# Kernel optimization log

Hardware: AMD Instinct MI355X
Metric: run time of the kernel (lower is better)

Reference implementation:

```python
import jax, jax.numpy as jnp
import numpy as np

N_NODES = 140000   # 14 frames * 10000 nodes/frame
N_EDGES = 2240000  # avg degree 16
NFEAT = 128
NHID = 128
N_FRAMES = 14


def setup_inputs() -> dict:
    key = jax.random.key(0)
    k1, k2, k3, k4, k5 = jax.random.split(key, 5)
    x = jax.random.normal(k1, (N_NODES, NFEAT), dtype=jnp.float32)
    # gc1 parameters (only layer actually used in forward)
    W = jax.random.normal(k2, (NFEAT, NHID), dtype=jnp.float32) * 0.05
    b = jnp.zeros((NHID,), dtype=jnp.float32)
    # sparse normalized adjacency as COO edge list (row sorted for fast segment_sum)
    edge_row = jnp.sort(jax.random.randint(k3, (N_EDGES,), 0, N_NODES, dtype=jnp.int32))
    edge_col = jax.random.randint(k4, (N_EDGES,), 0, N_NODES, dtype=jnp.int32)
    edge_val = jax.random.uniform(k5, (N_EDGES,), dtype=jnp.float32)
    return {"x": x, "W": W, "b": b, "edge_val": edge_val,
            "edge_row": edge_row, "edge_col": edge_col}


def reference(x, W, b, edge_val, edge_row, edge_col):
    # GraphConvolution: adj @ (x @ W) + b  (adj sparse, COO)
    support = x @ W                                   # [N, NHID]
    msgs = edge_val[:, None] * support[edge_col]      # [E, NHID] gather
    agg = jax.ops.segment_sum(msgs, edge_row, num_segments=N_NODES,
                              indices_are_sorted=True)  # [N, NHID] scatter-add
    h = jax.nn.relu(agg + b)
    # view(14, -1, c) then max over frame axis
    h = h.reshape(N_FRAMES, -1, NHID)                 # [14, N/14, NHID]
    h = jnp.max(h, axis=0)                            # [N/14, NHID]
    return jax.nn.log_softmax(h, axis=1)
```

## Files before the change

### kernel.cpp

```cpp
#include <hip/hip_runtime.h>
#include <hip/hip_bf16.h>

#define N_NODES 140000
#define N_EDGES 2240000
#define NFEAT 128
#define NHID 128
#define N_FRAMES 14
#define NODES_PER_FRAME 10000
#define CAP 352

typedef __attribute__((ext_vector_type(8))) short frag_b16;
typedef __attribute__((ext_vector_type(4))) int frag_i4;
typedef __attribute__((ext_vector_type(4))) float f32x4;

__device__ __forceinline__ unsigned short f2bf(float f) {
    union { float f; unsigned int u; } v; v.f = f;
    unsigned int r = v.u + 0x7fffu + ((v.u >> 16) & 1u);
    return (unsigned short)(r >> 16);
}
__device__ __forceinline__ int pk_bf16(float a, float b) {
    union { __hip_bfloat162 h; int i; } u;
    u.h = __float22bfloat162_rn(make_float2(a, b));
    return u.i;
}

__global__ void prep_kernel(const float* __restrict__ W, unsigned short* __restrict__ WT,
                            const int* __restrict__ edge_row, int* __restrict__ row_ptr) {
    int e = blockIdx.x * blockDim.x + threadIdx.x;
    if (e < NFEAT * NHID) {
        int k = e >> 7, n = e & 127;
        WT[n * 128 + k] = f2bf(W[e]);
    }
    if (e < N_EDGES) {
        int r = edge_row[e];
        int prev = (e == 0) ? -1 : edge_row[e - 1];
        for (int q = prev + 1; q <= r; ++q) row_ptr[q] = e;
        if (e == N_EDGES - 1) {
            for (int q = r + 1; q <= N_NODES; ++q) row_ptr[q] = N_EDGES;
        }
    }
}

#define WT_STRIDE 136

__global__ __launch_bounds__(256) void gemm_kernel(
        const float* __restrict__ x, const unsigned short* __restrict__ WT,
        unsigned char* __restrict__ supQ, float* __restrict__ scales) {
    __shared__ unsigned short wt_lds[128 * WT_STRIDE];

    const uint4* WTv = (const uint4*)WT;
    for (int idx = threadIdx.x; idx < 2048; idx += 256) {
        uint4 d = WTv[idx];
        int elem = idx << 3;
        int n = elem >> 7, k = elem & 127;
        *(uint4*)&wt_lds[n * WT_STRIDE + k] = d;
    }

    int wave = threadIdx.x >> 6;
    int lane = threadIdx.x & 63;
    int m = lane & 15;
    int q = lane >> 4;

    long row0 = (long)blockIdx.x * 64 + wave * 16;

    int arow = (int)row0 + m;
    if (arow >= N_NODES) arow = N_NODES - 1;
    const float* xrow = x + (long)arow * 128 + q * 8;
    frag_b16 xa[4];
#pragma unroll
    for (int ks = 0; ks < 4; ++ks) {
        float4 lo = *(const float4*)(xrow + ks * 32);
        float4 hi = *(const float4*)(xrow + ks * 32 + 4);
        union { frag_b16 f; frag_i4 i; } u;
        u.i[0] = pk_bf16(lo.x, lo.y);
        u.i[1] = pk_bf16(lo.z, lo.w);
        u.i[2] = pk_bf16(hi.x, hi.y);
        u.i[3] = pk_bf16(hi.z, hi.w);
        xa[ks] = u.f;
    }

    __syncthreads();

    if (row0 < N_NODES) {
        f32x4 acc[8];
#pragma unroll
        for (int t = 0; t < 8; ++t) acc[t] = (f32x4){0.f, 0.f, 0.f, 0.f};

#pragma unroll
        for (int t = 0; t < 8; ++t) {
            const unsigned short* bp = &wt_lds[(t * 16 + m) * WT_STRIDE + q * 8];
#pragma unroll
            for (int ks = 0; ks < 4; ++ks) {
                frag_b16 wfrag = *(const frag_b16*)(bp + ks * 32);
                acc[t] = __builtin_amdgcn_mfma_f32_16x16x32_bf16(wfrag, xa[ks], acc[t], 0, 0, 0);
            }
        }

        float amax = 0.f;
#pragma unroll
        for (int t = 0; t < 8; ++t)
#pragma unroll
            for (int r = 0; r < 4; ++r) amax = fmaxf(amax, fabsf(acc[t][r]));
        amax = fmaxf(amax, __shfl_xor(amax, 16));
        amax = fmaxf(amax, __shfl_xor(amax, 32));
        float rinv = amax > 0.f ? 127.f / amax : 0.f;

        long node = row0 + m;
        if (node < N_NODES) {
            if (q == 0) scales[node] = amax * (1.f / 127.f);
            unsigned char* srow = supQ + node * 128;
#pragma unroll
            for (int t = 0; t < 8; ++t) {
                unsigned u0 = (unsigned)(rintf(acc[t][0] * rinv) + 128.f);
                unsigned u1 = (unsigned)(rintf(acc[t][1] * rinv) + 128.f);
                unsigned u2 = (unsigned)(rintf(acc[t][2] * rinv) + 128.f);
                unsigned u3 = (unsigned)(rintf(acc[t][3] * rinv) + 128.f);
                *(unsigned*)(srow + t * 16 + q * 4) = u0 | (u1 << 8) | (u2 << 16) | (u3 << 24);
            }
        }
    }
}

__global__ __launch_bounds__(128) void agg_kernel(
        const unsigned char* __restrict__ supQ, const float* __restrict__ scales,
        const float* __restrict__ b,
        const float* __restrict__ edge_val, const int* __restrict__ edge_col,
        const int* __restrict__ row_ptr, float* __restrict__ out) {
    __shared__ int    segStart[2][8];
    __shared__ int    segLen[2][8];
    __shared__ int    segOff[2][8];
    __shared__ int2   eBuf[2][CAP];
    __shared__ float4 xch[2][32];

    const int i = blockIdx.x;
    const int lane = threadIdx.x & 63;
    const int w = threadIdx.x >> 6;
    const int eh = lane >> 5;
    const int f4 = lane & 31;
    const unsigned f4x4 = (unsigned)f4 * 4u;

    int a = 0, len = 0;
    if (lane < 7) {
        int n = (w * 7 + lane) * NODES_PER_FRAME + i;
        a = row_ptr[n];
        len = row_ptr[n + 1] - a;
    }
    int len8 = (len + 7) & ~7;
    int off = 0;
#pragma unroll
    for (int f2 = 0; f2 < 7; ++f2) {
        int L2 = __shfl(len8, f2);
        if (f2 < lane) off += L2;
    }
    if (lane < 7) { segStart[w][lane] = a; segLen[w][lane] = len; segOff[w][lane] = off; }
    if (lane == 6) segOff[w][7] = off + len8;
    __syncthreads();

    const bool fit = segOff[w][7] <= CAP;

    if (fit) {
#pragma unroll 1
        for (int f = 0; f < 7; ++f) {
            int g = segStart[w][f], s = segOff[w][f], L = segLen[w][f];
            int L8 = (L + 7) & ~7;
            for (int j = lane; j < L8; j += 64) {
                int2 v = make_int2(0, 0);
                if (j < L) {
                    int c = edge_col[g + j];
                    v.x = c;
                    v.y = __float_as_int(edge_val[g + j] * scales[c]);
                }
                eBuf[w][s + j] = v;
            }
        }
    }
    __syncthreads();

    const float4 bb = *(const float4*)&b[f4 * 4];
    float4 mx = make_float4(0.f, 0.f, 0.f, 0.f);

    if (fit) {
#pragma unroll 1
        for (int f = 0; f < 7; ++f) {
            int s = segOff[w][f];
            int e8 = s + ((segLen[w][f] + 7) & ~7);
            float a0 = 0.f, a1 = 0.f, a2 = 0.f, a3 = 0.f, svf = 0.f;
            for (int j = s; j < e8; j += 8) {
                int2 ed[4];
#pragma unroll
                for (int p = 0; p < 4; ++p) ed[p] = eBuf[w][j + 2 * p + eh];
                unsigned q4[4];
#pragma unroll
                for (int p = 0; p < 4; ++p)
                    q4[p] = *(const unsigned*)(supQ + (((unsigned)ed[p].x) << 7) + f4x4);
#pragma unroll
                for (int p = 0; p < 4; ++p) {
                    float vp = __int_as_float(ed[p].y);
                    a0 = fmaf(vp, (float)( q4[p]        & 0xffu), a0);
                    a1 = fmaf(vp, (float)((q4[p] >> 8)  & 0xffu), a1);
                    a2 = fmaf(vp, (float)((q4[p] >> 16) & 0xffu), a2);
                    a3 = fmaf(vp, (float)( q4[p] >> 24        ), a3);
                    svf += vp;
                }
            }
            a0 += __shfl_xor(a0, 32); a1 += __shfl_xor(a1, 32);
            a2 += __shfl_xor(a2, 32); a3 += __shfl_xor(a3, 32);
            svf += __shfl_xor(svf, 32);
            float h0 = fmaf(-128.f, svf, a0) + bb.x;
            float h1 = fmaf(-128.f, svf, a1) + bb.y;
            float h2 = fmaf(-128.f, svf, a2) + bb.z;
            float h3 = fmaf(-128.f, svf, a3) + bb.w;
            mx.x = fmaxf(mx.x, fmaxf(h0, 0.f));
            mx.y = fmaxf(mx.y, fmaxf(h1, 0.f));
            mx.z = fmaxf(mx.z, fmaxf(h2, 0.f));
            mx.w = fmaxf(mx.w, fmaxf(h3, 0.f));
        }
    } else {
#pragma unroll 1
        for (int f = 0; f < 7; ++f) {
            int g = segStart[w][f], L = segLen[w][f];
            float a0 = 0.f, a1 = 0.f, a2 = 0.f, a3 = 0.f, svf = 0.f;
            for (int j = eh; j < L; j += 2) {
                int c = edge_col[g + j];
                float vp = edge_val[g + j] * scales[c];
                unsigned qv = *(const unsigned*)(supQ + (((unsigned)c) << 7) + f4x4);
                a0 = fmaf(vp, (float)( qv        & 0xffu), a0);
                a1 = fmaf(vp, (float)((qv >> 8)  & 0xffu), a1);
                a2 = fmaf(vp, (float)((qv >> 16) & 0xffu), a2);
                a3 = fmaf(vp, (float)( qv >> 24        ), a3);
                svf += vp;
            }
            a0 += __shfl_xor(a0, 32); a1 += __shfl_xor(a1, 32);
            a2 += __shfl_xor(a2, 32); a3 += __shfl_xor(a3, 32);
            svf += __shfl_xor(svf, 32);
            float h0 = fmaf(-128.f, svf, a0) + bb.x;
            float h1 = fmaf(-128.f, svf, a1) + bb.y;
            float h2 = fmaf(-128.f, svf, a2) + bb.z;
            float h3 = fmaf(-128.f, svf, a3) + bb.w;
            mx.x = fmaxf(mx.x, fmaxf(h0, 0.f));
            mx.y = fmaxf(mx.y, fmaxf(h1, 0.f));
            mx.z = fmaxf(mx.z, fmaxf(h2, 0.f));
            mx.w = fmaxf(mx.w, fmaxf(h3, 0.f));
        }
    }

    if (eh == 0) xch[w][f4] = mx;
    __syncthreads();
    float4 m0 = xch[0][f4], m1 = xch[1][f4];
    float o0 = fmaxf(m0.x, m1.x);
    float o1 = fmaxf(m0.y, m1.y);
    float o2 = fmaxf(m0.z, m1.z);
    float o3 = fmaxf(m0.w, m1.w);

    float M = fmaxf(fmaxf(o0, o1), fmaxf(o2, o3));
#pragma unroll
    for (int o = 16; o >= 1; o >>= 1) M = fmaxf(M, __shfl_xor(M, o));
    float S = __expf(o0 - M) + __expf(o1 - M) + __expf(o2 - M) + __expf(o3 - M);
#pragma unroll
    for (int o = 16; o >= 1; o >>= 1) S += __shfl_xor(S, o);

    if (w == 0 && eh == 0) {
        float ls = __logf(S);
        *(float4*)&out[i * 128 + f4 * 4] =
            make_float4(o0 - M - ls, o1 - M - ls, o2 - M - ls, o3 - M - ls);
    }
}

extern "C" void kernel_launch(void* const* d_in, const int* in_sizes, int n_in,
                              void* d_out, int out_size, void* d_ws, size_t ws_size,
                              hipStream_t stream) {
    const float* x        = (const float*)d_in[0];
    const float* W        = (const float*)d_in[1];
    const float* b        = (const float*)d_in[2];
    const float* edge_val = (const float*)d_in[3];
    const int*   edge_row = (const int*)d_in[4];
    const int*   edge_col = (const int*)d_in[5];
    float* out = (float*)d_out;

    char* ws = (char*)d_ws;
    unsigned char*  supQ    = (unsigned char*)ws;
    float*          scales  = (float*)(ws + 17920000);
    unsigned short* WT      = (unsigned short*)(ws + 18480000);
    int*            row_ptr = (int*)(ws + 18512768);

    prep_kernel<<<(N_EDGES + 255) / 256, 256, 0, stream>>>(W, WT, edge_row, row_ptr);
    gemm_kernel<<<(N_NODES + 63) / 64, 256, 0, stream>>>(x, WT, supQ, scales);
    agg_kernel<<<NODES_PER_FRAME, 128, 0, stream>>>(supQ, scales, b, edge_val, edge_col, row_ptr, out);
}
```

Before: 200.3 us.

## Fuse prep into persistent GEMM kernel with register prefetch of x tiles

Merges the W transpose/bf16 conversion and the row_ptr build into the GEMM launch. Extra blocks past the GEMM grid build row_ptr, while the 1024 GEMM blocks each convert W directly into LDS and loop persistently over 16-row tiles. Each loop iteration prefetches the next tile's x rows into registers before running the MFMAs. This removes one kernel launch and the WT round trip through global memory, and overlaps x loads with compute. In exchange, every GEMM block now redoes the W conversion with scattered 2-byte LDS stores, and the fatter kernel may reduce occupancy.

```diff
diff --git a/kernel.cpp b/kernel.cpp
--- a/kernel.cpp
+++ b/kernel.cpp
@@ -9,6 +9,11 @@
 #define NODES_PER_FRAME 10000
 #define CAP 352
 
+#define N_TILES 8750
+#define GEMM_GRID 1024
+#define EDGE_BLOCKS ((N_EDGES + 255) / 256)
+#define WT_STRIDE 136
+
 typedef __attribute__((ext_vector_type(8))) short frag_b16;
 typedef __attribute__((ext_vector_type(4))) int frag_i4;
 typedef __attribute__((ext_vector_type(4))) float f32x4;
@@ -24,64 +29,76 @@
     return u.i;
 }
 
-__global__ void prep_kernel(const float* __restrict__ W, unsigned short* __restrict__ WT,
-                            const int* __restrict__ edge_row, int* __restrict__ row_ptr) {
-    int e = blockIdx.x * blockDim.x + threadIdx.x;
-    if (e < NFEAT * NHID) {
-        int k = e >> 7, n = e & 127;
-        WT[n * 128 + k] = f2bf(W[e]);
-    }
-    if (e < N_EDGES) {
-        int r = edge_row[e];
-        int prev = (e == 0) ? -1 : edge_row[e - 1];
-        for (int q = prev + 1; q <= r; ++q) row_ptr[q] = e;
-        if (e == N_EDGES - 1) {
-            for (int q = r + 1; q <= N_NODES; ++q) row_ptr[q] = N_EDGES;
-        }
-    }
-}
-
-#define WT_STRIDE 136
-
-__global__ __launch_bounds__(256) void gemm_kernel(
-        const float* __restrict__ x, const unsigned short* __restrict__ WT,
+__global__ __launch_bounds__(256, 4) void gemm_prep_kernel(
+        const float* __restrict__ x, const float* __restrict__ W,
+        const int* __restrict__ edge_row, int* __restrict__ row_ptr,
         unsigned char* __restrict__ supQ, float* __restrict__ scales) {
+
+    if (blockIdx.x >= GEMM_GRID) {
+        int e = (blockIdx.x - GEMM_GRID) * 256 + threadIdx.x;
+        if (e < N_EDGES) {
+            int r = edge_row[e];
+            int prev = (e == 0) ? -1 : edge_row[e - 1];
+            for (int q = prev + 1; q <= r; ++q) row_ptr[q] = e;
+            if (e == N_EDGES - 1) {
+                for (int q = r + 1; q <= N_NODES; ++q) row_ptr[q] = N_EDGES;
+            }
+        }
+        return;
+    }
+
     __shared__ unsigned short wt_lds[128 * WT_STRIDE];
 
-    const uint4* WTv = (const uint4*)WT;
-    for (int idx = threadIdx.x; idx < 2048; idx += 256) {
-        uint4 d = WTv[idx];
-        int elem = idx << 3;
-        int n = elem >> 7, k = elem & 127;
-        *(uint4*)&wt_lds[n * WT_STRIDE + k] = d;
-    }
-
-    int wave = threadIdx.x >> 6;
-    int lane = threadIdx.x & 63;
-    int m = lane & 15;
-    int q = lane >> 4;
-
-    long row0 = (long)blockIdx.x * 64 + wave * 16;
-
-    int arow = (int)row0 + m;
-    if (arow >= N_NODES) arow = N_NODES - 1;
-    const float* xrow = x + (long)arow * 128 + q * 8;
-    frag_b16 xa[4];
-#pragma unroll
-    for (int ks = 0; ks < 4; ++ks) {
-        float4 lo = *(const float4*)(xrow + ks * 32);
-        float4 hi = *(const float4*)(xrow + ks * 32 + 4);
-        union { frag_b16 f; frag_i4 i; } u;
-        u.i[0] = pk_bf16(lo.x, lo.y);
-        u.i[1] = pk_bf16(lo.z, lo.w);
-        u.i[2] = pk_bf16(hi.x, hi.y);
-        u.i[3] = pk_bf16(hi.z, hi.w);
-        xa[ks] = u.f;
-    }
-
+    const int wave = threadIdx.x >> 6;
+    const int lane = threadIdx.x & 63;
+    const int m = lane & 15;
+    const int q = lane >> 4;
+
+    int tile = blockIdx.x * 4 + wave;
+    float4 pf[8];
+    {
+        const float* xr = x + (long)(tile * 16 + m) * 128 + q * 8;
+#pragma unroll
+        for (int ks = 0; ks < 4; ++ks) {
+            pf[2 * ks]     = *(const float4*)(xr + ks * 32);
+            pf[2 * ks + 1] = *(const float4*)(xr + ks * 32 + 4);
+        }
+    }
+
+    for (int idx = threadIdx.x; idx < 4096; idx += 256) {
+        float4 wv = ((const float4*)W)[idx];
+        int k = idx >> 5;
+        int n = (idx & 31) << 2;
+        wt_lds[(n + 0) * WT_STRIDE + k] = f2bf(wv.x);
+        wt_lds[(n + 1) * WT_STRIDE + k] = f2bf(wv.y);
+        wt_lds[(n + 2) * WT_STRIDE + k] = f2bf(wv.z);
+        wt_lds[(n + 3) * WT_STRIDE + k] = f2bf(wv.w);
+    }
     __syncthreads();
 
-    if (row0 < N_NODES) {
+    for (;;) {
+        frag_b16 xa[4];
+#pragma unroll
+        for (int ks = 0; ks < 4; ++ks) {
+            union { frag_b16 f; frag_i4 i; } u;
+            u.i[0] = pk_bf16(pf[2 * ks].x, pf[2 * ks].y);
+            u.i[1] = pk_bf16(pf[2 * ks].z, pf[2 * ks].w);
+            u.i[2] = pk_bf16(pf[2 * ks + 1].x, pf[2 * ks + 1].y);
+            u.i[3] = pk_bf16(pf[2 * ks + 1].z, pf[2 * ks + 1].w);
+            xa[ks] = u.f;
+        }
+
+        const int next = tile + GEMM_GRID * 4;
+        const bool more = next < N_TILES;
+        if (more) {
+            const float* xr = x + (long)(next * 16 + m) * 128 + q * 8;
+#pragma unroll
+            for (int ks = 0; ks < 4; ++ks) {
+                pf[2 * ks]     = *(const float4*)(xr + ks * 32);
+                pf[2 * ks + 1] = *(const float4*)(xr + ks * 32 + 4);
+            }
+        }
+
         f32x4 acc[8];
 #pragma unroll
         for (int t = 0; t < 8; ++t) acc[t] = (f32x4){0.f, 0.f, 0.f, 0.f};
@@ -105,19 +122,20 @@
         amax = fmaxf(amax, __shfl_xor(amax, 32));
         float rinv = amax > 0.f ? 127.f / amax : 0.f;
 
-        long node = row0 + m;
-        if (node < N_NODES) {
-            if (q == 0) scales[node] = amax * (1.f / 127.f);
-            unsigned char* srow = supQ + node * 128;
-#pragma unroll
-            for (int t = 0; t < 8; ++t) {
-                unsigned u0 = (unsigned)(rintf(acc[t][0] * rinv) + 128.f);
-                unsigned u1 = (unsigned)(rintf(acc[t][1] * rinv) + 128.f);
-                unsigned u2 = (unsigned)(rintf(acc[t][2] * rinv) + 128.f);
-                unsigned u3 = (unsigned)(rintf(acc[t][3] * rinv) + 128.f);
-                *(unsigned*)(srow + t * 16 + q * 4) = u0 | (u1 << 8) | (u2 << 16) | (u3 << 24);
-            }
-        }
+        long node = (long)tile * 16 + m;
+        if (q == 0) scales[node] = amax * (1.f / 127.f);
+        unsigned char* srow = supQ + node * 128;
+#pragma unroll
+        for (int t = 0; t < 8; ++t) {
+            unsigned u0 = (unsigned)(rintf(acc[t][0] * rinv) + 128.f);
+            unsigned u1 = (unsigned)(rintf(acc[t][1] * rinv) + 128.f);
+            unsigned u2 = (unsigned)(rintf(acc[t][2] * rinv) + 128.f);
+            unsigned u3 = (unsigned)(rintf(acc[t][3] * rinv) + 128.f);
+            *(unsigned*)(srow + t * 16 + q * 4) = u0 | (u1 << 8) | (u2 << 16) | (u3 << 24);
+        }
+
+        if (!more) break;
+        tile = next;
     }
 }
 
@@ -280,10 +298,10 @@
     char* ws = (char*)d_ws;
     unsigned char*  supQ    = (unsigned char*)ws;
     float*          scales  = (float*)(ws + 17920000);
-    unsigned short* WT      = (unsigned short*)(ws + 18480000);
-    int*            row_ptr = (int*)(ws + 18512768);
-
-    prep_kernel<<<(N_EDGES + 255) / 256, 256, 0, stream>>>(W, WT, edge_row, row_ptr);
-    gemm_kernel<<<(N_NODES + 63) / 64, 256, 0, stream>>>(x, WT, supQ, scales);
-    agg_kernel<<<NODES_PER_FRAME, 128, 0, stream>>>(supQ, scales, b, edge_val, edge_col, row_ptr, out);
-}
+    int*            row_ptr = (int*)(ws + 18480000);
+
+    gemm_prep_kernel<<<GEMM_GRID + EDGE_BLOCKS, 256, 0, stream>>>(
+        x, W, edge_row, row_ptr, supQ, scales);
+    agg_kernel<<<NODES_PER_FRAME, 128, 0, stream>>>(
+        supQ, scales, b, edge_val, edge_col, row_ptr, out);
+}
```

New measurement: 252.4 us. +26.0%, slower.
